# Kernel optimization log

Hardware: AMD Instinct MI355X
Metric: run time of the kernel (lower is better)

## Reference

```python
import jax, jax.numpy as jnp
import numpy as np

N = 10000      # nodes
E = 320000     # edges
DIM = 256
HEADS = 8
HEAD_DIM = DIM // HEADS
EXP_HEADS = 16  # head_expand_scale=2.0 * heads
SCALE = HEAD_DIM ** -0.5


def setup_inputs() -> dict:
    key = jax.random.key(0)
    ks = jax.random.split(key, 12)
    w = lambda k, shp: (jax.random.normal(k, shp, dtype=jnp.float32) * 0.02)
    return {
        "x": jax.random.normal(ks[0], (N, DIM), dtype=jnp.float32),
        "edges": jax.random.normal(ks[1], (E, DIM), dtype=jnp.float32),
        "edge_index": jax.random.randint(ks[2], (2, E), 0, N, dtype=jnp.int32),
        "Wq": w(ks[3], (DIM, DIM)),
        "Wk": w(ks[4], (DIM, DIM)),
        "Wv": w(ks[5], (DIM, DIM)),
        "Wek": w(ks[6], (DIM, DIM)),
        "Wev": w(ks[7], (DIM, DIM)),
        "Wexp": w(ks[8], (EXP_HEADS, HEADS)),
        "Wsq": w(ks[9], (HEADS, EXP_HEADS)),
        "Wout": w(ks[10], (DIM, DIM)),
        "bout": jnp.zeros((DIM,), dtype=jnp.float32),
    }


def reference(x, edges, edge_index, Wq, Wk, Wv, Wek, Wev, Wexp, Wsq, Wout, bout):
    n = x.shape[0]
    dst = edge_index[0]  # softmax/scatter groups
    src = edge_index[1]  # gathered keys/values

    # node projections -> [n, h, d], then per-edge gather
    q = (x @ Wq.T).reshape(n, HEADS, HEAD_DIM)[dst]      # [e, h, d]
    k = (x @ Wk.T).reshape(n, HEADS, HEAD_DIM)[src]      # [e, h, d]
    v = (x @ Wv.T).reshape(n, HEADS, HEAD_DIM)[src]      # [e, h, d]

    # edge feature fusion
    ek = (edges @ Wek.T).reshape(-1, HEADS, HEAD_DIM)    # [e, h, d]
    ev = (edges @ Wev.T).reshape(-1, HEADS, HEAD_DIM)    # [e, h, d]

    k = (k + ek) * SCALE
    attn = jnp.einsum("ehd,ehd->eh", q, k)               # [e, h]

    # head expand -> GELU (exact, matching torch default) -> squeeze
    attn = jax.nn.gelu(attn @ Wexp.T, approximate=False) @ Wsq.T  # [e, h]

    # sparse softmax over edges grouped by destination node, per head
    m = jax.ops.segment_max(attn, dst, num_segments=n)   # [n, h]
    a = jnp.exp(attn - m[dst])
    s = jax.ops.segment_sum(a, dst, num_segments=n)      # [n, h]
    attn = a / (s[dst] + 1e-16)                          # [e, h]

    # weighted values scatter-summed to nodes
    out_e = attn[:, :, None] * (v + ev)                  # [e, h, d]
    out = jax.ops.segment_sum(out_e, dst, num_segments=n)  # [n, h, d]
    out = out.reshape(n, DIM) @ Wout.T + bout            # [n, dim]
    return out, attn
```

## Files before the change

kernel.cpp:

```cpp
#include <hip/hip_runtime.h>
#include <math.h>

typedef unsigned short u16;
typedef unsigned int u32;

#define DIM 256
#define HEADS 8
#define ATT_SCALE 0.17677669529663687f

__global__ void k_zero(int* hist, int n){
  int i = blockIdx.x*256 + threadIdx.x;
  if (i < n) hist[i] = 0;
}
__global__ void k_hist(const int* __restrict__ ei, int* __restrict__ hist, int ne){
  int e = blockIdx.x*256 + threadIdx.x;
  if (e < ne) atomicAdd(&hist[ei[e]], 1);
}
__global__ __launch_bounds__(256) void k_scan(const int* __restrict__ hist,
                                              int* __restrict__ rowptr,
                                              int* __restrict__ cursor, int n, int C){
  __shared__ int ssum[256];
  int t = threadIdx.x;
  int loc[64]; int sum = 0;
  for (int j=0;j<C;j++){
    int idx = t*C+j;
    int v = (idx < n) ? hist[idx] : 0;
    loc[j] = sum; sum += v;
  }
  ssum[t] = sum;
  __syncthreads();
  for (int off=1; off<256; off<<=1){
    int v = (t>=off) ? ssum[t-off] : 0;
    __syncthreads();
    ssum[t] += v;
    __syncthreads();
  }
  int base = ssum[t] - sum;
  for (int j=0;j<C;j++){
    int idx = t*C+j;
    if (idx <= n){
      int v = base + loc[j];
      rowptr[idx] = v;
      if (idx < n) cursor[idx] = v;
    }
  }
}
__global__ void k_scatter(const int* __restrict__ ei, int* __restrict__ cursor,
                          int* __restrict__ perm, int* __restrict__ ssrc, int ne){
  int e = blockIdx.x*256 + threadIdx.x;
  if (e < ne){
    int d = ei[e];
    int pos = atomicAdd(&cursor[d], 1);
    perm[pos] = e;
    ssrc[pos] = ei[ne + e];
  }
}

__global__ __launch_bounds__(256) void k_qkv_gemm(const float* __restrict__ x,
    const float* __restrict__ Wq, const float* __restrict__ Wk, const float* __restrict__ Wv,
    float* __restrict__ qkv, int N){
  __shared__ float As[32][64];
  __shared__ float Bs[32][64];
  int t = threadIdx.x;
  int i0 = blockIdx.x * 64;
  int bj = blockIdx.y;
  const float* W = (bj < 4) ? Wq : (bj < 8) ? Wk : Wv;
  int j0 = (bj & 3) * 64;
  int lr = t >> 2;
  int lk = (t & 3) * 8;
  int arow = i0 + lr; if (arow >= N) arow = N - 1;
  const float* ap = x + (size_t)arow*256 + lk;
  const float* bp = W + (size_t)(j0 + lr)*256 + lk;
  int tx = t & 15, ty = t >> 4;
  float acc[4][4] = {};
  for (int k0 = 0; k0 < 256; k0 += 32){
    float4 a0 = *(const float4*)(ap + k0);
    float4 a1 = *(const float4*)(ap + k0 + 4);
    float4 b0 = *(const float4*)(bp + k0);
    float4 b1 = *(const float4*)(bp + k0 + 4);
    __syncthreads();
    As[lk+0][lr]=a0.x; As[lk+1][lr]=a0.y; As[lk+2][lr]=a0.z; As[lk+3][lr]=a0.w;
    As[lk+4][lr]=a1.x; As[lk+5][lr]=a1.y; As[lk+6][lr]=a1.z; As[lk+7][lr]=a1.w;
    Bs[lk+0][lr]=b0.x; Bs[lk+1][lr]=b0.y; Bs[lk+2][lr]=b0.z; Bs[lk+3][lr]=b0.w;
    Bs[lk+4][lr]=b1.x; Bs[lk+5][lr]=b1.y; Bs[lk+6][lr]=b1.z; Bs[lk+7][lr]=b1.w;
    __syncthreads();
    #pragma unroll
    for (int k = 0; k < 32; k++){
      float4 a = *(const float4*)&As[k][ty*4];
      float4 b = *(const float4*)&Bs[k][tx*4];
      float av[4] = {a.x, a.y, a.z, a.w};
      float bv[4] = {b.x, b.y, b.z, b.w};
      #pragma unroll
      for (int m = 0; m < 4; m++)
        #pragma unroll
        for (int n = 0; n < 4; n++)
          acc[m][n] += av[m] * bv[n];
    }
  }
  #pragma unroll
  for (int m = 0; m < 4; m++){
    int row = i0 + ty*4 + m;
    if (row < N){
      float4 o; o.x = acc[m][0]; o.y = acc[m][1]; o.z = acc[m][2]; o.w = acc[m][3];
      *(float4*)(qkv + (size_t)row*768 + bj*64 + tx*4) = o;
    }
  }
}

__global__ __launch_bounds__(256) void k_transpose2(const float* __restrict__ Wev,
    const float* __restrict__ Wout, float* __restrict__ WevT, float* __restrict__ WoutT){
  __shared__ float tile[32][33];
  const float* src = blockIdx.z ? Wout : Wev;
  float*       dst = blockIdx.z ? WoutT : WevT;
  int bx = blockIdx.x * 32, by = blockIdx.y * 32;
  int tx = threadIdx.x & 31, ty4 = (threadIdx.x >> 5) * 4;
  #pragma unroll
  for (int r = 0; r < 4; r++)
    tile[ty4+r][tx] = src[(size_t)(by + ty4 + r)*256 + bx + tx];
  __syncthreads();
  #pragma unroll
  for (int r = 0; r < 4; r++)
    dst[(size_t)(bx + ty4 + r)*256 + by + tx] = tile[tx][ty4+r];
}

__global__ __launch_bounds__(256) void k_attn(
    const float* __restrict__ qkv, const float* __restrict__ Wek,
    const float* __restrict__ edges, const float* __restrict__ Wexp, const float* __restrict__ Wsq,
    const int* __restrict__ rowptr, const int* __restrict__ perm, const int* __restrict__ ssrc,
    float* __restrict__ zbuf, float* __restrict__ attn_out){
  __shared__ float g_s[8][260];
  __shared__ float q_s[256];
  __shared__ float we_s[128];
  __shared__ float wsq_s[128];
  __shared__ float es_s[8][256];
  __shared__ int  src_s[8];
  __shared__ float z_s[8][8];
  __shared__ float t_s[8][16];
  __shared__ float z2_s[8][8];
  __shared__ float m_s[8];
  __shared__ float s_s[8];
  int i = blockIdx.x, t = threadIdx.x;
  int rs = rowptr[i], re = rowptr[i+1];
  q_s[t] = qkv[(size_t)i*768 + t];
  if (t < 128) we_s[t] = Wexp[t];
  else         wsq_s[t-128] = Wsq[t-128];
  __syncthreads();
  #pragma unroll
  for (int h=0;h<8;h++){
    float a = 0.f;
    #pragma unroll
    for (int d=0; d<32; d++){
      a += q_s[h*32+d] * Wek[(size_t)(h*32+d)*256 + t];
    }
    g_s[h][t] = a;
  }
  __syncthreads();
  int h = t>>5, s = t&31;
  float mreg = -3.0e38f;
  for (int p0 = rs; p0 < re; p0 += 8){
    int nE = min(8, re-p0);
    for (int ee=0; ee<nE; ee++){
      int er = perm[p0+ee];
      es_s[ee][t] = edges[(size_t)er*256 + t];
    }
    if (t < nE) src_s[t] = ssrc[p0+t];
    __syncthreads();
    for (int ee=0; ee<nE; ee++){
      float partial = 0.f;
      #pragma unroll
      for (int j=0;j<8;j++) partial += es_s[ee][s*8+j]*g_s[h][s*8+j];
      partial += q_s[h*32+s] * qkv[(size_t)src_s[ee]*768 + 256 + h*32 + s];
      #pragma unroll
      for (int off=16; off>=1; off>>=1)
        partial += __shfl_xor(partial, off, 32);
      if (s == 0) z_s[ee][h] = partial * ATT_SCALE;
    }
    __syncthreads();
    if (t < nE*16){
      int ee = t>>4, j = t&15;
      float u = 0.f;
      #pragma unroll
      for (int hh=0;hh<8;hh++) u += z_s[ee][hh]*we_s[j*8+hh];
      u = 0.5f*u*(1.f + erff(u*0.70710678118654752f));
      t_s[ee][j] = u;
    }
    __syncthreads();
    if (t < nE*8){
      int ee = t>>3, hh = t&7;
      float z2 = 0.f;
      #pragma unroll
      for (int j=0;j<16;j++) z2 += t_s[ee][j]*wsq_s[hh*16+j];
      z2_s[ee][hh] = z2;
      zbuf[(size_t)(p0+ee)*8 + hh] = z2;
    }
    __syncthreads();
    if (t < 8){
      for (int ee=0;ee<nE;ee++) mreg = fmaxf(mreg, z2_s[ee][t]);
    }
    __syncthreads();
  }
  if (t < 8) m_s[t] = mreg;
  __syncthreads();
  if (t < 8){
    float sr = 0.f;
    for (int p=rs; p<re; p++) sr += expf(zbuf[(size_t)p*8 + t] - m_s[t]);
    s_s[t] = sr;
  }
  __syncthreads();
  {
    int pp = t>>3, hh = t&7;
    for (int p = rs+pp; p < re; p += 32){
      float z = zbuf[(size_t)p*8 + hh];
      float a = expf(z - m_s[hh]) / (s_s[hh] + 1e-16f);
      zbuf[(size_t)p*8 + hh] = a;
      attn_out[(size_t)perm[p]*8 + hh] = a;
    }
  }
}

template<bool COALESCED>
__global__ __launch_bounds__(256) void k_out(
    const float* __restrict__ qkv, const float* __restrict__ edges,
    const float* __restrict__ Wv_, const float* __restrict__ Wo_, const float* __restrict__ bout,
    const int* __restrict__ rowptr, const int* __restrict__ perm, const int* __restrict__ ssrc,
    const float* __restrict__ zbuf, float* __restrict__ out_d){
  __shared__ float es_s[8][256];
  __shared__ float a_s[8][8];
  __shared__ int  src_s[8];
  __shared__ float t_s[8][260];
  __shared__ float o_s[256];
  int i = blockIdx.x, t = threadIdx.x;
  int rs = rowptr[i], re = rowptr[i+1];
  int hc = t>>5;
  float tacc[8];
  #pragma unroll
  for (int j=0;j<8;j++) tacc[j]=0.f;
  float vacc = 0.f;
  for (int p0=rs; p0<re; p0+=8){
    int nE = min(8, re-p0);
    for (int ee=0; ee<nE; ee++){
      int er = perm[p0+ee];
      es_s[ee][t] = edges[(size_t)er*256 + t];
    }
    if (t < nE*8) a_s[t>>3][t&7] = zbuf[(size_t)(p0 + (t>>3))*8 + (t&7)];
    if (t < nE)   src_s[t] = ssrc[p0+t];
    __syncthreads();
    for (int ee=0; ee<nE; ee++){
      float ef = es_s[ee][t];
      #pragma unroll
      for (int j=0;j<8;j++) tacc[j] += a_s[ee][j]*ef;
      vacc += a_s[ee][hc] * qkv[(size_t)src_s[ee]*768 + 512 + t];
    }
    __syncthreads();
  }
  #pragma unroll
  for (int j=0;j<8;j++) t_s[j][t] = tacc[j];
  __syncthreads();
  float vtot = vacc;
  {
    const float* tp = &t_s[hc][0];
    if (COALESCED){
      for (int c=0;c<256;c++) vtot += Wv_[(size_t)c*256 + t]*tp[c];
    } else {
      const float* wp = Wv_ + (size_t)t*256;
      for (int c=0;c<256;c++) vtot += wp[c]*tp[c];
    }
  }
  o_s[t] = vtot;
  __syncthreads();
  float oacc = bout[t];
  if (COALESCED){
    for (int c=0;c<256;c++) oacc += Wo_[(size_t)c*256 + t]*o_s[c];
  } else {
    const float* wp = Wo_ + (size_t)t*256;
    for (int c=0;c<256;c++) oacc += wp[c]*o_s[c];
  }
  out_d[(size_t)i*256 + t] = oacc;
}

extern "C" void kernel_launch(void* const* d_in, const int* in_sizes, int n_in,
                              void* d_out, int out_size, void* d_ws, size_t ws_size,
                              hipStream_t stream){
  const float* x     = (const float*)d_in[0];
  const float* edges = (const float*)d_in[1];
  const int*   ei    = (const int*)d_in[2];
  const float* Wq    = (const float*)d_in[3];
  const float* Wk    = (const float*)d_in[4];
  const float* Wv    = (const float*)d_in[5];
  const float* Wek   = (const float*)d_in[6];
  const float* Wev   = (const float*)d_in[7];
  const float* Wexp  = (const float*)d_in[8];
  const float* Wsq   = (const float*)d_in[9];
  const float* Wout  = (const float*)d_in[10];
  const float* bout  = (const float*)d_in[11];

  const int N = in_sizes[0] / DIM;
  const int E = in_sizes[2] / 2;

  char* base = (char*)d_ws;
  size_t off = 0;
  auto align256 = [](size_t v){ return (v + 255) & ~(size_t)255; };
  float* qkv    = (float*)(base + off); off += align256((size_t)N*768*4);
  float* zbuf   = (float*)(base + off); off += align256((size_t)E*8*4);
  int*   rowptr = (int*)(base + off);   off += align256((size_t)(N+1)*4);
  int*   cursor = (int*)(base + off);   off += align256((size_t)N*4);
  int*   hist   = (int*)(base + off);   off += align256((size_t)N*4);
  int*   perm   = (int*)(base + off);   off += align256((size_t)E*4);
  int*   ssrc   = (int*)(base + off);   off += align256((size_t)E*4);
  size_t off_tr = off;
  float* WevT   = (float*)(base + off_tr);
  float* WoutT  = (float*)(base + off_tr + align256((size_t)256*256*4));
  size_t off_end = off_tr + 2*align256((size_t)256*256*4);
  const bool use_tr = (off_end <= ws_size);

  float* out_d  = (float*)d_out;
  float* attn_d = out_d + (size_t)N*DIM;

  int C = N/256 + 1;
  if (C > 64) C = 64;

  k_zero<<<(N+255)/256, 256, 0, stream>>>(hist, N);
  k_hist<<<(E+255)/256, 256, 0, stream>>>(ei, hist, E);
  k_scan<<<1, 256, 0, stream>>>(hist, rowptr, cursor, N, C);
  k_scatter<<<(E+255)/256, 256, 0, stream>>>(ei, cursor, perm, ssrc, E);
  if (use_tr)
    k_transpose2<<<dim3(8,8,2), 256, 0, stream>>>(Wev, Wout, WevT, WoutT);
  dim3 g_qkv((N+63)/64, 12);
  k_qkv_gemm<<<g_qkv, 256, 0, stream>>>(x, Wq, Wk, Wv, qkv, N);
  k_attn<<<N, 256, 0, stream>>>(qkv, Wek, edges, Wexp, Wsq,
                                rowptr, perm, ssrc, zbuf, attn_d);
  if (use_tr)
    k_out<true><<<N, 256, 0, stream>>>(qkv, edges, WevT, WoutT, bout,
                                       rowptr, perm, ssrc, zbuf, out_d);
  else
    k_out<false><<<N, 256, 0, stream>>>(qkv, edges, Wev, Wout, bout,
                                        rowptr, perm, ssrc, zbuf, out_d);
}
```

Before: 1.213 ms.

## Fuse attention and output kernels with online softmax and prefetched edge rows

Merges the attention-score kernel and the output aggregation kernel into one per-node kernel. Softmax runs online, rescaling the accumulators by the change in running max, so edge features are read from global memory once instead of twice. The next chunk's edge rows are prefetched into registers as float4 loads, and the K/V rows of the source nodes are loaded together per chunk. In exchange the kernel uses more registers and shared memory, which may lower occupancy, and the online rescaling adds some extra work.

```diff
diff --git a/kernel.cpp b/kernel.cpp
--- a/kernel.cpp
+++ b/kernel.cpp
@@ -123,142 +123,163 @@
     dst[(size_t)(bx + ty4 + r)*256 + by + tx] = tile[tx][ty4+r];
 }
 
-__global__ __launch_bounds__(256) void k_attn(
+template<bool COALESCED>
+__global__ __launch_bounds__(256) void k_fused(
     const float* __restrict__ qkv, const float* __restrict__ Wek,
     const float* __restrict__ edges, const float* __restrict__ Wexp, const float* __restrict__ Wsq,
+    const float* __restrict__ Wv_, const float* __restrict__ Wo_, const float* __restrict__ bout,
     const int* __restrict__ rowptr, const int* __restrict__ perm, const int* __restrict__ ssrc,
-    float* __restrict__ zbuf, float* __restrict__ attn_out){
+    float* __restrict__ zbuf, float* __restrict__ attn_out, float* __restrict__ out_d){
   __shared__ float g_s[8][260];
   __shared__ float q_s[256];
   __shared__ float we_s[128];
   __shared__ float wsq_s[128];
-  __shared__ float es_s[8][256];
-  __shared__ int  src_s[8];
+  __shared__ float pool[8][260];
+  __shared__ int   src_s[8];
   __shared__ float z_s[8][8];
-  __shared__ float t_s[8][16];
+  __shared__ float t16_s[8][16];
   __shared__ float z2_s[8][8];
+  __shared__ float a_s[8][8];
   __shared__ float m_s[8];
   __shared__ float s_s[8];
+  __shared__ float r_s[8];
+  __shared__ float o_s[256];
+
   int i = blockIdx.x, t = threadIdx.x;
   int rs = rowptr[i], re = rowptr[i+1];
+  int h = t>>5, s = t&31;
+
   q_s[t] = qkv[(size_t)i*768 + t];
   if (t < 128) we_s[t] = Wexp[t];
   else         wsq_s[t-128] = Wsq[t-128];
-  __syncthreads();
-  #pragma unroll
-  for (int h=0;h<8;h++){
+  if (t < 8){ m_s[t] = -3.0e38f; s_s[t] = 0.f; }
+  __syncthreads();
+  #pragma unroll
+  for (int hh=0; hh<8; hh++){
     float a = 0.f;
     #pragma unroll
-    for (int d=0; d<32; d++){
-      a += q_s[h*32+d] * Wek[(size_t)(h*32+d)*256 + t];
-    }
-    g_s[h][t] = a;
-  }
-  __syncthreads();
-  int h = t>>5, s = t&31;
-  float mreg = -3.0e38f;
+    for (int d=0; d<32; d++)
+      a += q_s[hh*32+d] * Wek[(size_t)(hh*32+d)*256 + t];
+    g_s[hh][t] = a;
+  }
+
+  const float4* e4 = (const float4*)edges;
+  int r0 = t>>6, c40 = t&63;
+  int r1 = r0 + 4;
+  float4 c0, c1;
+  if (re - rs >= 8){
+    int ea = perm[rs + r0], eb = perm[rs + r1];
+    c0 = e4[(size_t)ea*64 + c40];
+    c1 = e4[(size_t)eb*64 + c40];
+  }
+  __syncthreads();
+
+  float tacc[8];
+  #pragma unroll
+  for (int j=0;j<8;j++) tacc[j]=0.f;
+  float vacc = 0.f;
+
   for (int p0 = rs; p0 < re; p0 += 8){
     int nE = min(8, re-p0);
+    if (nE == 8){
+      *(float4*)&pool[r0][c40*4] = c0;
+      *(float4*)&pool[r1][c40*4] = c1;
+      if (re - (p0+8) >= 8){
+        int ea = perm[p0+8 + r0], eb = perm[p0+8 + r1];
+        c0 = e4[(size_t)ea*64 + c40];
+        c1 = e4[(size_t)eb*64 + c40];
+      }
+    } else {
+      for (int ee=0; ee<nE; ee++){
+        int er = perm[p0+ee];
+        pool[ee][t] = edges[(size_t)er*256 + t];
+      }
+    }
+    if (t < nE) src_s[t] = ssrc[p0+t];
+    __syncthreads();
+
+    float kreg[8], vreg[8];
+    for (int ee=0; ee<nE; ee++) kreg[ee] = qkv[(size_t)src_s[ee]*768 + 256 + t];
+    for (int ee=0; ee<nE; ee++) vreg[ee] = qkv[(size_t)src_s[ee]*768 + 512 + t];
+
     for (int ee=0; ee<nE; ee++){
-      int er = perm[p0+ee];
-      es_s[ee][t] = edges[(size_t)er*256 + t];
-    }
-    if (t < nE) src_s[t] = ssrc[p0+t];
-    __syncthreads();
-    for (int ee=0; ee<nE; ee++){
-      float partial = 0.f;
-      #pragma unroll
-      for (int j=0;j<8;j++) partial += es_s[ee][s*8+j]*g_s[h][s*8+j];
-      partial += q_s[h*32+s] * qkv[(size_t)src_s[ee]*768 + 256 + h*32 + s];
+      float partial = q_s[t] * kreg[ee];
+      #pragma unroll
+      for (int j=0;j<8;j++) partial += pool[ee][j*32+s]*g_s[h][j*32+s];
       #pragma unroll
       for (int off=16; off>=1; off>>=1)
         partial += __shfl_xor(partial, off, 32);
       if (s == 0) z_s[ee][h] = partial * ATT_SCALE;
     }
     __syncthreads();
+
     if (t < nE*16){
       int ee = t>>4, j = t&15;
       float u = 0.f;
       #pragma unroll
       for (int hh=0;hh<8;hh++) u += z_s[ee][hh]*we_s[j*8+hh];
       u = 0.5f*u*(1.f + erff(u*0.70710678118654752f));
-      t_s[ee][j] = u;
-    }
-    __syncthreads();
+      t16_s[ee][j] = u;
+    }
+    __syncthreads();
+
     if (t < nE*8){
       int ee = t>>3, hh = t&7;
       float z2 = 0.f;
       #pragma unroll
-      for (int j=0;j<16;j++) z2 += t_s[ee][j]*wsq_s[hh*16+j];
+      for (int j=0;j<16;j++) z2 += t16_s[ee][j]*wsq_s[hh*16+j];
       z2_s[ee][hh] = z2;
       zbuf[(size_t)(p0+ee)*8 + hh] = z2;
     }
     __syncthreads();
+
     if (t < 8){
-      for (int ee=0;ee<nE;ee++) mreg = fmaxf(mreg, z2_s[ee][t]);
-    }
-    __syncthreads();
-  }
-  if (t < 8) m_s[t] = mreg;
-  __syncthreads();
-  if (t < 8){
-    float sr = 0.f;
-    for (int p=rs; p<re; p++) sr += expf(zbuf[(size_t)p*8 + t] - m_s[t]);
-    s_s[t] = sr;
-  }
-  __syncthreads();
+      float cm = -3.0e38f;
+      for (int ee=0; ee<nE; ee++) cm = fmaxf(cm, z2_s[ee][t]);
+      float mo = m_s[t];
+      float mn = fmaxf(mo, cm);
+      float r  = expf(mo - mn);
+      float sa = 0.f;
+      for (int ee=0; ee<nE; ee++){
+        float a = expf(z2_s[ee][t] - mn);
+        a_s[ee][t] = a; sa += a;
+      }
+      s_s[t] = s_s[t]*r + sa;
+      m_s[t] = mn;
+      r_s[t] = r;
+    }
+    __syncthreads();
+
+    float rh = r_s[h];
+    vacc *= rh;
+    for (int ee=0; ee<nE; ee++) vacc += a_s[ee][h]*vreg[ee];
+    #pragma unroll
+    for (int j=0;j<8;j++) tacc[j] *= r_s[j];
+    for (int ee=0; ee<nE; ee++){
+      float ef = pool[ee][t];
+      #pragma unroll
+      for (int j=0;j<8;j++) tacc[j] += a_s[ee][j]*ef;
+    }
+    __syncthreads();
+  }
+
+  #pragma unroll
+  for (int j=0;j<8;j++) tacc[j] = tacc[j] / (s_s[j] + 1e-16f);
+  float vnorm = vacc / (s_s[h] + 1e-16f);
+  #pragma unroll
+  for (int j=0;j<8;j++) pool[j][t] = tacc[j];
+  __syncthreads();
+
   {
     int pp = t>>3, hh = t&7;
-    for (int p = rs+pp; p < re; p += 32){
-      float z = zbuf[(size_t)p*8 + hh];
-      float a = expf(z - m_s[hh]) / (s_s[hh] + 1e-16f);
-      zbuf[(size_t)p*8 + hh] = a;
-      attn_out[(size_t)perm[p]*8 + hh] = a;
-    }
-  }
-}
-
-template<bool COALESCED>
-__global__ __launch_bounds__(256) void k_out(
-    const float* __restrict__ qkv, const float* __restrict__ edges,
-    const float* __restrict__ Wv_, const float* __restrict__ Wo_, const float* __restrict__ bout,
-    const int* __restrict__ rowptr, const int* __restrict__ perm, const int* __restrict__ ssrc,
-    const float* __restrict__ zbuf, float* __restrict__ out_d){
-  __shared__ float es_s[8][256];
-  __shared__ float a_s[8][8];
-  __shared__ int  src_s[8];
-  __shared__ float t_s[8][260];
-  __shared__ float o_s[256];
-  int i = blockIdx.x, t = threadIdx.x;
-  int rs = rowptr[i], re = rowptr[i+1];
-  int hc = t>>5;
-  float tacc[8];
-  #pragma unroll
-  for (int j=0;j<8;j++) tacc[j]=0.f;
-  float vacc = 0.f;
-  for (int p0=rs; p0<re; p0+=8){
-    int nE = min(8, re-p0);
-    for (int ee=0; ee<nE; ee++){
-      int er = perm[p0+ee];
-      es_s[ee][t] = edges[(size_t)er*256 + t];
-    }
-    if (t < nE*8) a_s[t>>3][t&7] = zbuf[(size_t)(p0 + (t>>3))*8 + (t&7)];
-    if (t < nE)   src_s[t] = ssrc[p0+t];
-    __syncthreads();
-    for (int ee=0; ee<nE; ee++){
-      float ef = es_s[ee][t];
-      #pragma unroll
-      for (int j=0;j<8;j++) tacc[j] += a_s[ee][j]*ef;
-      vacc += a_s[ee][hc] * qkv[(size_t)src_s[ee]*768 + 512 + t];
-    }
-    __syncthreads();
-  }
-  #pragma unroll
-  for (int j=0;j<8;j++) t_s[j][t] = tacc[j];
-  __syncthreads();
-  float vtot = vacc;
+    float mh = m_s[hh], shv = s_s[hh] + 1e-16f;
+    for (int p = rs+pp; p < re; p += 32)
+      attn_out[(size_t)perm[p]*8 + hh] = expf(zbuf[(size_t)p*8 + hh] - mh) / shv;
+  }
+
+  float vtot = vnorm;
   {
-    const float* tp = &t_s[hc][0];
+    const float* tp = &pool[h][0];
     if (COALESCED){
       for (int c=0;c<256;c++) vtot += Wv_[(size_t)c*256 + t]*tp[c];
     } else {
@@ -327,12 +348,12 @@
     k_transpose2<<<dim3(8,8,2), 256, 0, stream>>>(Wev, Wout, WevT, WoutT);
   dim3 g_qkv((N+63)/64, 12);
   k_qkv_gemm<<<g_qkv, 256, 0, stream>>>(x, Wq, Wk, Wv, qkv, N);
-  k_attn<<<N, 256, 0, stream>>>(qkv, Wek, edges, Wexp, Wsq,
-                                rowptr, perm, ssrc, zbuf, attn_d);
   if (use_tr)
-    k_out<true><<<N, 256, 0, stream>>>(qkv, edges, WevT, WoutT, bout,
-                                       rowptr, perm, ssrc, zbuf, out_d);
+    k_fused<true><<<N, 256, 0, stream>>>(qkv, Wek, edges, Wexp, Wsq,
+                                         WevT, WoutT, bout,
+                                         rowptr, perm, ssrc, zbuf, attn_d, out_d);
   else
-    k_out<false><<<N, 256, 0, stream>>>(qkv, edges, Wev, Wout, bout,
-                                        rowptr, perm, ssrc, zbuf, out_d);
-}
+    k_fused<false><<<N, 256, 0, stream>>>(qkv, Wek, edges, Wexp, Wsq,
+                                          Wev, Wout, bout,
+                                          rowptr, perm, ssrc, zbuf, attn_d, out_d);
+}
```

After: 1.088 ms. -10.3%, faster.
